# Kernel optimization log

Hardware: AMD Instinct MI355X
Metric: run time of the kernel (lower is better)

Reference implementation:

```python
import jax, jax.numpy as jnp
import numpy as np

GRID = 16  # int(sqrt(num_patches=256))
# fixed ragged grid shapes: 32 images cycling through 4 aspect ratios
_SHAPES = np.array([[32, 32], [16, 64], [24, 40], [40, 24]] * 8, dtype=np.int64)  # [32,2]
_SIZES = _SHAPES[:, 0] * _SHAPES[:, 1]  # per-image patch counts
_SEQ_LEN = int(_SIZES.sum())  # 31744


def setup_inputs() -> dict:
    key = jax.random.key(0)
    k1, k2, k3 = jax.random.split(key, 3)
    return {
        "seq_patches": jax.random.normal(k1, (_SEQ_LEN, 768), dtype=jnp.float32),
        "w": jax.random.normal(k2, (1152, 768), dtype=jnp.float32) * 0.02,
        "b": jnp.zeros((1152,), dtype=jnp.float32),
        "pos_emb": jax.random.normal(k3, (256, 1152), dtype=jnp.float32) * 0.02,
        "seq_sizes": jnp.asarray(_SIZES),
        "spatial_shapes": jnp.asarray(_SHAPES),
    }


def reference(seq_patches, w, b, pos_emb, seq_sizes, spatial_shapes):
    # Linear patch embedding: [S, 768] @ [768, 1152] + [1152]
    patch_embeds = seq_patches @ w.T + b
    d = pos_emb.shape[-1]
    pos_grid = pos_emb.reshape(GRID, GRID, d)  # [16,16,D]
    shapes = np.asarray(spatial_shapes)  # static host-side shapes (ragged loop)
    pos_list = []
    for h, wd in shapes:
        # antialiased bilinear resize, half-pixel centers (align_corners=False)
        rp = jax.image.resize(pos_grid, (int(h), int(wd), d), method="linear", antialias=True)
        pos_list.append(rp.reshape(int(h) * int(wd), d))
    pos_embeds = jnp.concatenate(pos_list, axis=0)  # [S, D]
    return patch_embeds + pos_embeds
```

## Files before the change

### kernel.cpp

```cpp
#include <hip/hip_runtime.h>
#include <hip/hip_bf16.h>
#include <cstdint>
#include <cstddef>

typedef __attribute__((ext_vector_type(8))) short short8;
typedef __attribute__((ext_vector_type(4))) float f32x4;

static constexpr int M_TOT = 31744;
static constexpr int N_TOT = 1152;
static constexpr int K_TOT = 768;
static constexpr long A_ELEMS = (long)M_TOT * K_TOT;
static constexpr long W_ELEMS = (long)N_TOT * K_TOT;
static constexpr int CYC_ROWS = 3968;

__device__ __forceinline__ unsigned short f2bf(float f) {
  unsigned int u = __float_as_uint(f);
  u += 0x7FFFu + ((u >> 16) & 1u);
  return (unsigned short)(u >> 16);
}
__device__ __forceinline__ float bf2f(unsigned short u) {
  return __uint_as_float((unsigned int)u << 16);
}

__global__ void cvt_kernel(const float* __restrict__ A, const float* __restrict__ W,
                           unsigned short* __restrict__ dst) {
  long chunk = (long)blockIdx.x * blockDim.x + threadIdx.x;
  long i = chunk * 8;
  const float* src = (i < A_ELEMS) ? (A + i) : (W + (i - A_ELEMS));
  float4 v0 = *(const float4*)(src);
  float4 v1 = *(const float4*)(src + 4);
  short8 o;
  o[0] = (short)f2bf(v0.x); o[1] = (short)f2bf(v0.y);
  o[2] = (short)f2bf(v0.z); o[3] = (short)f2bf(v0.w);
  o[4] = (short)f2bf(v1.x); o[5] = (short)f2bf(v1.y);
  o[6] = (short)f2bf(v1.z); o[7] = (short)f2bf(v1.w);
  *(short8*)(dst + i) = o;
}

__global__ void tab_kernel(const float* __restrict__ pos, const float* __restrict__ bias,
                           unsigned short* __restrict__ tab) {
  const int t = blockIdx.x * blockDim.x + threadIdx.x;
  const int row = t / 144;
  const int dc = (t - row * 144) * 8;

  int rr, cc; float sy, sx;
  if (row < 1024)      { rr = row >> 5; cc = row & 31; sy = 0.5f;         sx = 0.5f; }
  else if (row < 2048) { const int li = row - 1024; rr = li >> 6; cc = li & 63; sy = 1.0f; sx = 0.25f; }
  else if (row < 3008) { const int li = row - 2048; rr = li / 40; cc = li - rr * 40; sy = 16.0f / 24.0f; sx = 0.4f; }
  else                 { const int li = row - 3008; rr = li / 24; cc = li - rr * 24; sy = 0.4f; sx = 16.0f / 24.0f; }
  float yc = fminf(fmaxf(((float)rr + 0.5f) * sy - 0.5f, 0.0f), 15.0f);
  const int y0 = (int)yc; const float fy = yc - (float)y0;
  const int y1 = y0 < 15 ? y0 + 1 : 15;
  float xc = fminf(fmaxf(((float)cc + 0.5f) * sx - 0.5f, 0.0f), 15.0f);
  const int x0 = (int)xc; const float fx = xc - (float)x0;
  const int x1 = x0 < 15 ? x0 + 1 : 15;
  const float w11 = fy * fx;
  const float w10 = fy - w11;
  const float w01 = fx - w11;
  const float w00 = 1.0f - fy - fx + w11;
  const float* p00 = pos + (size_t)(y0 * 16 + x0) * 1152 + dc;
  const float* p01 = pos + (size_t)(y0 * 16 + x1) * 1152 + dc;
  const float* p10 = pos + (size_t)(y1 * 16 + x0) * 1152 + dc;
  const float* p11 = pos + (size_t)(y1 * 16 + x1) * 1152 + dc;
  const float* bi  = bias + dc;
  short8 o;
#pragma unroll
  for (int j = 0; j < 8; ++j) {
    const float v = bi[j] + w00 * p00[j] + w01 * p01[j] + w10 * p10[j] + w11 * p11[j];
    o[j] = (short)f2bf(v);
  }
  *(short8*)(tab + (size_t)row * 1152 + dc) = o;
}

__device__ __forceinline__ void gload_lds16(const void* g, void* l) {
  __builtin_amdgcn_global_load_lds((__attribute__((address_space(1))) void*)g,
                                   (__attribute__((address_space(3))) void*)l, 16, 0, 0);
}

__global__ __launch_bounds__(256) void gemm_kernel(
    const unsigned short* __restrict__ Abf, const unsigned short* __restrict__ Wbf,
    const unsigned short* __restrict__ tab, float* __restrict__ outp) {
  __shared__ __attribute__((aligned(16))) unsigned short As[3][128 * 32];
  __shared__ __attribute__((aligned(16))) unsigned short Bs[3][128 * 32];

  const int bid = blockIdx.x;
  const int tile = (bid & 7) * 279 + (bid >> 3);
  const int tm = tile / 9, tn = tile % 9;
  const int m0 = tm * 128, n0 = tn * 128;

  const int tid = threadIdx.x;
  const int wid = tid >> 6, lane = tid & 63;
  const int wr = wid >> 1, wc = wid & 1;
  const int kg = lane >> 4, l15 = lane & 15;

  const int srow = lane >> 2;
  const int schunk = ((lane & 3) ^ ((lane >> 3) & 3)) * 8;
  const unsigned short* Abase = Abf + (size_t)(m0 + wid * 16 + srow) * K_TOT + schunk;
  const unsigned short* Bbase = Wbf + (size_t)(n0 + wid * 16 + srow) * K_TOT + schunk;
  const int wu = wid << 10;

  const int rkey = (l15 >> 1) & 3;

  f32x4 acc[4][4] = {};

#define STAGE(p, kt)                                                             \
  { const int k0_ = (kt) * 32;                                                   \
    gload_lds16(Abase + k0_,                      (char*)As[p] + wu);            \
    gload_lds16(Abase + (size_t)64 * K_TOT + k0_, (char*)As[p] + 4096 + wu);     \
    gload_lds16(Bbase + k0_,                      (char*)Bs[p] + wu);            \
    gload_lds16(Bbase + (size_t)64 * K_TOT + k0_, (char*)Bs[p] + 4096 + wu); }

#define COMPUTE(p)                                                               \
  { __builtin_amdgcn_s_setprio(1);                                               \
    short8 fa[4], fb[4];                                                         \
    _Pragma("unroll") for (int m = 0; m < 4; ++m) {                              \
      const int arow = wr * 64 + m * 16 + l15;                                   \
      fa[m] = *(const short8*)((const char*)As[p] + arow * 64 +                  \
                               ((kg ^ rkey) << 4));                              \
    }                                                                            \
    _Pragma("unroll") for (int n = 0; n < 4; ++n) {                              \
      const int brow = wc * 64 + n * 16 + l15;                                   \
      fb[n] = *(const short8*)((const char*)Bs[p] + brow * 64 +                  \
                               ((kg ^ rkey) << 4));                              \
    }                                                                            \
    _Pragma("unroll") for (int m = 0; m < 4; ++m)                                \
      _Pragma("unroll") for (int n = 0; n < 4; ++n)                              \
        acc[m][n] = __builtin_amdgcn_mfma_f32_16x16x32_bf16(                     \
            fa[m], fb[n], acc[m][n], 0, 0, 0);                                   \
    __builtin_amdgcn_s_setprio(0); }

  STAGE(0, 0)
  STAGE(1, 1)

#pragma unroll
  for (int t = 0; t < 24; ++t) {
    const int p = t % 3;
    if (t + 2 < 24) {
      STAGE((t + 2) % 3, t + 2)
      asm volatile("s_waitcnt vmcnt(8)" ::: "memory");
    } else if (t + 1 < 24) {
      asm volatile("s_waitcnt vmcnt(4)" ::: "memory");
    } else {
      asm volatile("s_waitcnt vmcnt(0)" ::: "memory");
    }
    __builtin_amdgcn_s_barrier();
    COMPUTE(p)
    __builtin_amdgcn_s_barrier();
  }

#undef STAGE
#undef COMPUTE

  const int s_base = m0 + wr * 64 + ((lane >> 4) << 2);
  const int rem_base = s_base % CYC_ROWS;
  const int d_base = n0 + wc * 64 + l15;

#pragma unroll
  for (int m = 0; m < 4; ++m) {
#pragma unroll
    for (int r = 0; r < 4; ++r) {
      const int off = m * 16 + r;
      int rem = rem_base + off;
      if (rem >= CYC_ROWS) rem -= CYC_ROWS;
      const unsigned short* trow = tab + (size_t)rem * 1152 + d_base;
      float* orow = outp + (size_t)(s_base + off) * 1152 + d_base;
#pragma unroll
      for (int n = 0; n < 4; ++n)
        orow[n * 16] = acc[m][n][r] + bf2f(trow[n * 16]);
    }
  }
}

extern "C" void kernel_launch(void* const* d_in, const int* in_sizes, int n_in,
                              void* d_out, int out_size, void* d_ws, size_t ws_size,
                              hipStream_t stream) {
  const float* A    = (const float*)d_in[0];
  const float* W    = (const float*)d_in[1];
  const float* bias = (const float*)d_in[2];
  const float* pos  = (const float*)d_in[3];
  unsigned short* Abf = (unsigned short*)d_ws;
  unsigned short* Wbf = Abf + A_ELEMS;
  unsigned short* tab = Wbf + W_ELEMS;
  float* outp = (float*)d_out;

  cvt_kernel<<<12336, 256, 0, stream>>>(A, W, Abf);
  tab_kernel<<<2232, 256, 0, stream>>>(pos, bias, tab);
  gemm_kernel<<<2232, 256, 0, stream>>>(Abf, Wbf, tab, outp);
}
```

Baseline: 117.0 us.

## Enlarge GEMM tile to 256x128 with per-wave 128x64 outputs

```diff
diff --git a/kernel.cpp b/kernel.cpp
--- a/kernel.cpp
+++ b/kernel.cpp
@@ -77,56 +77,57 @@
                                    (__attribute__((address_space(3))) void*)l, 16, 0, 0);
 }
 
-__global__ __launch_bounds__(256) void gemm_kernel(
+__global__ __launch_bounds__(256, 2) void gemm_kernel(
     const unsigned short* __restrict__ Abf, const unsigned short* __restrict__ Wbf,
     const unsigned short* __restrict__ tab, float* __restrict__ outp) {
-  __shared__ __attribute__((aligned(16))) unsigned short As[3][128 * 32];
+  __shared__ __attribute__((aligned(16))) unsigned short As[3][256 * 32];
   __shared__ __attribute__((aligned(16))) unsigned short Bs[3][128 * 32];
 
   const int bid = blockIdx.x;
-  const int tile = (bid & 7) * 279 + (bid >> 3);
-  const int tm = tile / 9, tn = tile % 9;
-  const int m0 = tm * 128, n0 = tn * 128;
+  const int xcd = bid & 7, idx = bid >> 3;
+  const int wgid = (xcd < 4 ? xcd * 140 : 560 + (xcd - 4) * 139) + idx;
+  const int tm = wgid / 9, tn = wgid - tm * 9;
+  const int m0 = tm * 256, n0 = tn * 128;
 
   const int tid = threadIdx.x;
-  const int wid = tid >> 6, lane = tid & 63;
-  const int wr = wid >> 1, wc = wid & 1;
+  const int w = tid >> 6, lane = tid & 63;
+  const int wm = w >> 1, wn = w & 1;
   const int kg = lane >> 4, l15 = lane & 15;
 
   const int srow = lane >> 2;
   const int schunk = ((lane & 3) ^ ((lane >> 3) & 3)) * 8;
-  const unsigned short* Abase = Abf + (size_t)(m0 + wid * 16 + srow) * K_TOT + schunk;
-  const unsigned short* Bbase = Wbf + (size_t)(n0 + wid * 16 + srow) * K_TOT + schunk;
-  const int wu = wid << 10;
+  const unsigned short* Abase = Abf + (size_t)(m0 + w * 64 + srow) * K_TOT + schunk;
+  const unsigned short* Bbase = Wbf + (size_t)(n0 + w * 32 + srow) * K_TOT + schunk;
 
   const int rkey = (l15 >> 1) & 3;
 
-  f32x4 acc[4][4] = {};
+  f32x4 acc[8][4] = {};
 
-#define STAGE(p, kt)                                                             \
+#define STAGE(p_, kt)                                                            \
   { const int k0_ = (kt) * 32;                                                   \
-    gload_lds16(Abase + k0_,                      (char*)As[p] + wu);            \
-    gload_lds16(Abase + (size_t)64 * K_TOT + k0_, (char*)As[p] + 4096 + wu);     \
-    gload_lds16(Bbase + k0_,                      (char*)Bs[p] + wu);            \
-    gload_lds16(Bbase + (size_t)64 * K_TOT + k0_, (char*)Bs[p] + 4096 + wu); }
+    gload_lds16(Abase + k0_,                      (char*)As[p_] + (w * 64) * 64);      \
+    gload_lds16(Abase + (size_t)16 * K_TOT + k0_, (char*)As[p_] + (w * 64 + 16) * 64); \
+    gload_lds16(Abase + (size_t)32 * K_TOT + k0_, (char*)As[p_] + (w * 64 + 32) * 64); \
+    gload_lds16(Abase + (size_t)48 * K_TOT + k0_, (char*)As[p_] + (w * 64 + 48) * 64); \
+    gload_lds16(Bbase + k0_,                      (char*)Bs[p_] + (w * 32) * 64);      \
+    gload_lds16(Bbase + (size_t)16 * K_TOT + k0_, (char*)Bs[p_] + (w * 32 + 16) * 64); }
 
-#define COMPUTE(p)                                                               \
+#define COMPUTE(p_)                                                              \
   { __builtin_amdgcn_s_setprio(1);                                               \
-    short8 fa[4], fb[4];                                                         \
-    _Pragma("unroll") for (int m = 0; m < 4; ++m) {                              \
-      const int arow = wr * 64 + m * 16 + l15;                                   \
-      fa[m] = *(const short8*)((const char*)As[p] + arow * 64 +                  \
+    short8 fb[4];                                                                \
+    _Pragma("unroll") for (int n = 0; n < 4; ++n) {                              \
+      const int br_ = wn * 64 + n * 16 + l15;                                    \
+      fb[n] = *(const short8*)((const char*)Bs[p_] + br_ * 64 +                  \
                                ((kg ^ rkey) << 4));                              \
     }                                                                            \
-    _Pragma("unroll") for (int n = 0; n < 4; ++n) {                              \
-      const int brow = wc * 64 + n * 16 + l15;                                   \
-      fb[n] = *(const short8*)((const char*)Bs[p] + brow * 64 +                  \
-                               ((kg ^ rkey) << 4));                              \
+    _Pragma("unroll") for (int i = 0; i < 8; ++i) {                              \
+      const int ar_ = wm * 128 + i * 16 + l15;                                   \
+      const short8 fa_ = *(const short8*)((const char*)As[p_] + ar_ * 64 +       \
+                                          ((kg ^ rkey) << 4));                   \
+      _Pragma("unroll") for (int n = 0; n < 4; ++n)                              \
+        acc[i][n] = __builtin_amdgcn_mfma_f32_16x16x32_bf16(                     \
+            fa_, fb[n], acc[i][n], 0, 0, 0);                                     \
     }                                                                            \
-    _Pragma("unroll") for (int m = 0; m < 4; ++m)                                \
-      _Pragma("unroll") for (int n = 0; n < 4; ++n)                              \
-        acc[m][n] = __builtin_amdgcn_mfma_f32_16x16x32_bf16(                     \
-            fa[m], fb[n], acc[m][n], 0, 0, 0);                                   \
     __builtin_amdgcn_s_setprio(0); }
 
   STAGE(0, 0)
@@ -135,11 +136,11 @@
 #pragma unroll
   for (int t = 0; t < 24; ++t) {
     const int p = t % 3;
-    if (t + 2 < 24) {
+    if (t < 22) {
       STAGE((t + 2) % 3, t + 2)
-      asm volatile("s_waitcnt vmcnt(8)" ::: "memory");
-    } else if (t + 1 < 24) {
-      asm volatile("s_waitcnt vmcnt(4)" ::: "memory");
+      asm volatile("s_waitcnt vmcnt(12)" ::: "memory");
+    } else if (t == 22) {
+      asm volatile("s_waitcnt vmcnt(6)" ::: "memory");
     } else {
       asm volatile("s_waitcnt vmcnt(0)" ::: "memory");
     }
@@ -151,22 +152,22 @@
 #undef STAGE
 #undef COMPUTE
 
-  const int s_base = m0 + wr * 64 + ((lane >> 4) << 2);
+  const int s_base = m0 + wm * 128 + ((lane >> 4) << 2);
   const int rem_base = s_base % CYC_ROWS;
-  const int d_base = n0 + wc * 64 + l15;
+  const int d_base = n0 + wn * 64 + l15;
 
 #pragma unroll
-  for (int m = 0; m < 4; ++m) {
+  for (int i = 0; i < 8; ++i) {
 #pragma unroll
     for (int r = 0; r < 4; ++r) {
-      const int off = m * 16 + r;
+      const int off = i * 16 + r;
       int rem = rem_base + off;
       if (rem >= CYC_ROWS) rem -= CYC_ROWS;
       const unsigned short* trow = tab + (size_t)rem * 1152 + d_base;
       float* orow = outp + (size_t)(s_base + off) * 1152 + d_base;
 #pragma unroll
       for (int n = 0; n < 4; ++n)
-        orow[n * 16] = acc[m][n][r] + bf2f(trow[n * 16]);
+        orow[n * 16] = acc[i][n][r] + bf2f(trow[n * 16]);
     }
   }
 }
@@ -185,5 +186,5 @@
 
   cvt_kernel<<<12336, 256, 0, stream>>>(A, W, Abf);
   tab_kernel<<<2232, 256, 0, stream>>>(pos, bias, tab);
-  gemm_kernel<<<2232, 256, 0, stream>>>(Abf, Wbf, tab, outp);
+  gemm_kernel<<<1116, 256, 0, stream>>>(Abf, Wbf, tab, outp);
 }
```

After: 129.9 us. 11.1% more time.

## Give each wave private LDS tiles to drop block barriers, fuse prep kernels

Applied to the files above, without the earlier changes.

```diff
diff --git a/kernel.cpp b/kernel.cpp
--- a/kernel.cpp
+++ b/kernel.cpp
@@ -22,24 +22,24 @@
   return __uint_as_float((unsigned int)u << 16);
 }
 
-__global__ void cvt_kernel(const float* __restrict__ A, const float* __restrict__ W,
-                           unsigned short* __restrict__ dst) {
-  long chunk = (long)blockIdx.x * blockDim.x + threadIdx.x;
-  long i = chunk * 8;
-  const float* src = (i < A_ELEMS) ? (A + i) : (W + (i - A_ELEMS));
-  float4 v0 = *(const float4*)(src);
-  float4 v1 = *(const float4*)(src + 4);
-  short8 o;
-  o[0] = (short)f2bf(v0.x); o[1] = (short)f2bf(v0.y);
-  o[2] = (short)f2bf(v0.z); o[3] = (short)f2bf(v0.w);
-  o[4] = (short)f2bf(v1.x); o[5] = (short)f2bf(v1.y);
-  o[6] = (short)f2bf(v1.z); o[7] = (short)f2bf(v1.w);
-  *(short8*)(dst + i) = o;
-}
-
-__global__ void tab_kernel(const float* __restrict__ pos, const float* __restrict__ bias,
-                           unsigned short* __restrict__ tab) {
-  const int t = blockIdx.x * blockDim.x + threadIdx.x;
+__global__ void prep_kernel(const float* __restrict__ A, const float* __restrict__ W,
+                            const float* __restrict__ pos, const float* __restrict__ bias,
+                            unsigned short* __restrict__ dst, unsigned short* __restrict__ tab) {
+  const int b = blockIdx.x;
+  if (b < 12336) {
+    long i = ((long)b * 256 + threadIdx.x) * 8;
+    const float* src = (i < A_ELEMS) ? (A + i) : (W + (i - A_ELEMS));
+    float4 v0 = *(const float4*)(src);
+    float4 v1 = *(const float4*)(src + 4);
+    short8 o;
+    o[0] = (short)f2bf(v0.x); o[1] = (short)f2bf(v0.y);
+    o[2] = (short)f2bf(v0.z); o[3] = (short)f2bf(v0.w);
+    o[4] = (short)f2bf(v1.x); o[5] = (short)f2bf(v1.y);
+    o[6] = (short)f2bf(v1.z); o[7] = (short)f2bf(v1.w);
+    *(short8*)(dst + i) = o;
+    return;
+  }
+  const int t = (b - 12336) * 256 + threadIdx.x;
   const int row = t / 144;
   const int dc = (t - row * 144) * 8;
 
@@ -77,11 +77,10 @@
                                    (__attribute__((address_space(3))) void*)l, 16, 0, 0);
 }
 
-__global__ __launch_bounds__(256) void gemm_kernel(
+__global__ __launch_bounds__(256, 2) void gemm_kernel(
     const unsigned short* __restrict__ Abf, const unsigned short* __restrict__ Wbf,
     const unsigned short* __restrict__ tab, float* __restrict__ outp) {
-  __shared__ __attribute__((aligned(16))) unsigned short As[3][128 * 32];
-  __shared__ __attribute__((aligned(16))) unsigned short Bs[3][128 * 32];
+  __shared__ __attribute__((aligned(16))) unsigned short Lds[2 * 4 * 4096];
 
   const int bid = blockIdx.x;
   const int tile = (bid & 7) * 279 + (bid >> 3);
@@ -89,40 +88,41 @@
   const int m0 = tm * 128, n0 = tn * 128;
 
   const int tid = threadIdx.x;
-  const int wid = tid >> 6, lane = tid & 63;
-  const int wr = wid >> 1, wc = wid & 1;
+  const int w = tid >> 6, lane = tid & 63;
+  const int wr = w >> 1, wc = w & 1;
   const int kg = lane >> 4, l15 = lane & 15;
 
   const int srow = lane >> 2;
   const int schunk = ((lane & 3) ^ ((lane >> 3) & 3)) * 8;
-  const unsigned short* Abase = Abf + (size_t)(m0 + wid * 16 + srow) * K_TOT + schunk;
-  const unsigned short* Bbase = Wbf + (size_t)(n0 + wid * 16 + srow) * K_TOT + schunk;
-  const int wu = wid << 10;
+  const unsigned short* Asrc = Abf + (size_t)(m0 + wr * 64 + srow) * K_TOT + schunk;
+  const unsigned short* Bsrc = Wbf + (size_t)(n0 + wc * 64 + srow) * K_TOT + schunk;
+  char* const myLds = (char*)Lds + w * 8192;
 
   const int rkey = (l15 >> 1) & 3;
 
   f32x4 acc[4][4] = {};
 
-#define STAGE(p, kt)                                                             \
-  { const int k0_ = (kt) * 32;                                                   \
-    gload_lds16(Abase + k0_,                      (char*)As[p] + wu);            \
-    gload_lds16(Abase + (size_t)64 * K_TOT + k0_, (char*)As[p] + 4096 + wu);     \
-    gload_lds16(Bbase + k0_,                      (char*)Bs[p] + wu);            \
-    gload_lds16(Bbase + (size_t)64 * K_TOT + k0_, (char*)Bs[p] + 4096 + wu); }
+#define STAGE(p_, kt)                                                            \
+  { char* rg_ = myLds + (p_) * 32768;                                            \
+    const int k0_ = (kt) * 32;                                                   \
+    gload_lds16(Asrc + k0_,                      rg_);                           \
+    gload_lds16(Asrc + (size_t)16 * K_TOT + k0_, rg_ + 1024);                    \
+    gload_lds16(Asrc + (size_t)32 * K_TOT + k0_, rg_ + 2048);                    \
+    gload_lds16(Asrc + (size_t)48 * K_TOT + k0_, rg_ + 3072);                    \
+    gload_lds16(Bsrc + k0_,                      rg_ + 4096);                    \
+    gload_lds16(Bsrc + (size_t)16 * K_TOT + k0_, rg_ + 5120);                    \
+    gload_lds16(Bsrc + (size_t)32 * K_TOT + k0_, rg_ + 6144);                    \
+    gload_lds16(Bsrc + (size_t)48 * K_TOT + k0_, rg_ + 7168); }
 
-#define COMPUTE(p)                                                               \
-  { __builtin_amdgcn_s_setprio(1);                                               \
+#define COMPUTE(p_)                                                              \
+  { const char* rg_ = myLds + (p_) * 32768;                                      \
     short8 fa[4], fb[4];                                                         \
-    _Pragma("unroll") for (int m = 0; m < 4; ++m) {                              \
-      const int arow = wr * 64 + m * 16 + l15;                                   \
-      fa[m] = *(const short8*)((const char*)As[p] + arow * 64 +                  \
+    _Pragma("unroll") for (int m = 0; m < 4; ++m)                                \
+      fa[m] = *(const short8*)(rg_ + (m * 16 + l15) * 64 + ((kg ^ rkey) << 4));  \
+    _Pragma("unroll") for (int n = 0; n < 4; ++n)                                \
+      fb[n] = *(const short8*)(rg_ + 4096 + (n * 16 + l15) * 64 +                \
                                ((kg ^ rkey) << 4));                              \
-    }                                                                            \
-    _Pragma("unroll") for (int n = 0; n < 4; ++n) {                              \
-      const int brow = wc * 64 + n * 16 + l15;                                   \
-      fb[n] = *(const short8*)((const char*)Bs[p] + brow * 64 +                  \
-                               ((kg ^ rkey) << 4));                              \
-    }                                                                            \
+    __builtin_amdgcn_s_setprio(1);                                               \
     _Pragma("unroll") for (int m = 0; m < 4; ++m)                                \
       _Pragma("unroll") for (int n = 0; n < 4; ++n)                              \
         acc[m][n] = __builtin_amdgcn_mfma_f32_16x16x32_bf16(                     \
@@ -130,22 +130,17 @@
     __builtin_amdgcn_s_setprio(0); }
 
   STAGE(0, 0)
-  STAGE(1, 1)
 
-#pragma unroll
   for (int t = 0; t < 24; ++t) {
-    const int p = t % 3;
-    if (t + 2 < 24) {
-      STAGE((t + 2) % 3, t + 2)
+    const int p = t & 1;
+    __builtin_amdgcn_sched_barrier(0);
+    if (t < 23) {
+      STAGE(p ^ 1, t + 1)
       asm volatile("s_waitcnt vmcnt(8)" ::: "memory");
-    } else if (t + 1 < 24) {
-      asm volatile("s_waitcnt vmcnt(4)" ::: "memory");
     } else {
       asm volatile("s_waitcnt vmcnt(0)" ::: "memory");
     }
-    __builtin_amdgcn_s_barrier();
     COMPUTE(p)
-    __builtin_amdgcn_s_barrier();
   }
 
 #undef STAGE
@@ -183,7 +178,6 @@
   unsigned short* tab = Wbf + W_ELEMS;
   float* outp = (float*)d_out;
 
-  cvt_kernel<<<12336, 256, 0, stream>>>(A, W, Abf);
-  tab_kernel<<<2232, 256, 0, stream>>>(pos, bias, tab);
+  prep_kernel<<<14568, 256, 0, stream>>>(A, W, pos, bias, Abf, tab);
   gemm_kernel<<<2232, 256, 0, stream>>>(Abf, Wbf, tab, outp);
 }
```

New measurement: 142.5 us. 1.22x slower.

## Load B fragments directly to registers, deepen A LDS pipeline to four stages

Applied to the files above, without the earlier changes.

```diff
diff --git a/kernel.cpp b/kernel.cpp
--- a/kernel.cpp
+++ b/kernel.cpp
@@ -77,11 +77,10 @@
                                    (__attribute__((address_space(3))) void*)l, 16, 0, 0);
 }
 
-__global__ __launch_bounds__(256) void gemm_kernel(
+__global__ __launch_bounds__(256, 3) void gemm_kernel(
     const unsigned short* __restrict__ Abf, const unsigned short* __restrict__ Wbf,
     const unsigned short* __restrict__ tab, float* __restrict__ outp) {
-  __shared__ __attribute__((aligned(16))) unsigned short As[3][128 * 32];
-  __shared__ __attribute__((aligned(16))) unsigned short Bs[3][128 * 32];
+  __shared__ __attribute__((aligned(16))) unsigned short As[4][128 * 32];
 
   const int bid = blockIdx.x;
   const int tile = (bid & 7) * 279 + (bid >> 3);
@@ -96,59 +95,65 @@
   const int srow = lane >> 2;
   const int schunk = ((lane & 3) ^ ((lane >> 3) & 3)) * 8;
   const unsigned short* Abase = Abf + (size_t)(m0 + wid * 16 + srow) * K_TOT + schunk;
-  const unsigned short* Bbase = Wbf + (size_t)(n0 + wid * 16 + srow) * K_TOT + schunk;
   const int wu = wid << 10;
+
+  const unsigned short* Bfrag = Wbf + (size_t)(n0 + wc * 64 + l15) * K_TOT + kg * 8;
 
   const int rkey = (l15 >> 1) & 3;
 
   f32x4 acc[4][4] = {};
+  short8 fbtA[4], fbtB[4];
 
-#define STAGE(p, kt)                                                             \
+#define BLOAD(dst_, kt)                                                          \
+  _Pragma("unroll") for (int n = 0; n < 4; ++n)                                  \
+    dst_[n] = *(const short8*)(Bfrag + (size_t)(n * 16) * K_TOT + (kt) * 32);
+
+#define STAGE_A(p_, kt)                                                          \
   { const int k0_ = (kt) * 32;                                                   \
-    gload_lds16(Abase + k0_,                      (char*)As[p] + wu);            \
-    gload_lds16(Abase + (size_t)64 * K_TOT + k0_, (char*)As[p] + 4096 + wu);     \
-    gload_lds16(Bbase + k0_,                      (char*)Bs[p] + wu);            \
-    gload_lds16(Bbase + (size_t)64 * K_TOT + k0_, (char*)Bs[p] + 4096 + wu); }
+    gload_lds16(Abase + k0_,                      (char*)As[p_] + wu);           \
+    gload_lds16(Abase + (size_t)64 * K_TOT + k0_, (char*)As[p_] + 4096 + wu); }
 
-#define COMPUTE(p)                                                               \
+#define COMPUTE(p_, fb_)                                                         \
   { __builtin_amdgcn_s_setprio(1);                                               \
-    short8 fa[4], fb[4];                                                         \
+    short8 fa[4];                                                                \
     _Pragma("unroll") for (int m = 0; m < 4; ++m) {                              \
-      const int arow = wr * 64 + m * 16 + l15;                                   \
-      fa[m] = *(const short8*)((const char*)As[p] + arow * 64 +                  \
-                               ((kg ^ rkey) << 4));                              \
-    }                                                                            \
-    _Pragma("unroll") for (int n = 0; n < 4; ++n) {                              \
-      const int brow = wc * 64 + n * 16 + l15;                                   \
-      fb[n] = *(const short8*)((const char*)Bs[p] + brow * 64 +                  \
+      const int ar_ = wr * 64 + m * 16 + l15;                                    \
+      fa[m] = *(const short8*)((const char*)As[p_] + ar_ * 64 +                  \
                                ((kg ^ rkey) << 4));                              \
     }                                                                            \
     _Pragma("unroll") for (int m = 0; m < 4; ++m)                                \
       _Pragma("unroll") for (int n = 0; n < 4; ++n)                              \
         acc[m][n] = __builtin_amdgcn_mfma_f32_16x16x32_bf16(                     \
-            fa[m], fb[n], acc[m][n], 0, 0, 0);                                   \
+            fa[m], fb_[n], acc[m][n], 0, 0, 0);                                  \
     __builtin_amdgcn_s_setprio(0); }
 
-  STAGE(0, 0)
-  STAGE(1, 1)
+  BLOAD(fbtA, 0)
+  STAGE_A(0, 0)
+  STAGE_A(1, 1)
+  STAGE_A(2, 2)
+  asm volatile("s_waitcnt vmcnt(4)" ::: "memory");
+  __builtin_amdgcn_s_barrier();
 
 #pragma unroll
   for (int t = 0; t < 24; ++t) {
-    const int p = t % 3;
-    if (t + 2 < 24) {
-      STAGE((t + 2) % 3, t + 2)
-      asm volatile("s_waitcnt vmcnt(8)" ::: "memory");
-    } else if (t + 1 < 24) {
-      asm volatile("s_waitcnt vmcnt(4)" ::: "memory");
-    } else {
-      asm volatile("s_waitcnt vmcnt(0)" ::: "memory");
+    const int p = t & 3;
+    if (t < 23) {
+      if (t & 1) { BLOAD(fbtA, t + 1) } else { BLOAD(fbtB, t + 1) }
     }
-    __builtin_amdgcn_s_barrier();
-    COMPUTE(p)
+    if (t < 21) STAGE_A((t + 3) & 3, t + 3)
+    if (t > 0) {
+      if (t < 21)       { asm volatile("s_waitcnt vmcnt(8)" ::: "memory"); }
+      else if (t == 21) { asm volatile("s_waitcnt vmcnt(6)" ::: "memory"); }
+      else if (t == 22) { asm volatile("s_waitcnt vmcnt(4)" ::: "memory"); }
+      else              { asm volatile("s_waitcnt vmcnt(0)" ::: "memory"); }
+      __builtin_amdgcn_s_barrier();
+    }
+    if (t & 1) { COMPUTE(p, fbtB) } else { COMPUTE(p, fbtA) }
     __builtin_amdgcn_s_barrier();
   }
 
-#undef STAGE
+#undef BLOAD
+#undef STAGE_A
 #undef COMPUTE
 
   const int s_base = m0 + wr * 64 + ((lane >> 4) << 2);
```

New measurement: 168.0 us. 1.44x slower.
